# Kernel tuning notes

Hardware: AMD Instinct MI355X
Metric: run time of the kernel (lower is better)

The kernel has to match this reference:

```python
import jax, jax.numpy as jnp
import numpy as np
from jax import lax

NUM_MASKS = 100
NUM_CLASSES = 81  # 80 + 1
KERNEL_DIM = 256
BIAS_PRIOR = float(-np.log((1 - 0.01) / 0.01))


def setup_inputs() -> dict:
    key = jax.random.key(0)
    ks = jax.random.split(key, 12)
    B, C, H, W = 4, 256, 160, 160
    D = C  # expand_dim = in_channels * num_groups
    inp = {
        "features": jax.random.normal(ks[0], (B, C, H, W), jnp.float32),
        # iam_conv: Conv2d(C, num_masks, 3, padding=1)
        "w_iam": jax.random.normal(ks[1], (NUM_MASKS, C, 3, 3), jnp.float32) * 0.01,
        "b_iam": jnp.full((NUM_MASKS,), BIAS_PRIOR, jnp.float32),
        "softmax_bias": jnp.ones((1,), jnp.float32),
        # fc: Linear(D, D), xavier-ish
        "w_fc": jax.random.normal(ks[2], (D, D), jnp.float32) * (1.0 / np.sqrt(D)),
        "b_fc": jnp.zeros((D,), jnp.float32),
        "w_cls": jax.random.normal(ks[3], (NUM_CLASSES, D), jnp.float32) * 0.01,
        "b_cls": jnp.full((NUM_CLASSES,), BIAS_PRIOR, jnp.float32),
        "w_ker": jax.random.normal(ks[4], (KERNEL_DIM, D), jnp.float32) * 0.01,
        "b_ker": jnp.zeros((KERNEL_DIM,), jnp.float32),
        "w_obj": jax.random.normal(ks[5], (1, D), jnp.float32) * (1.0 / np.sqrt(D)),
        "b_obj": jnp.zeros((1,), jnp.float32),
        "w_box": jax.random.normal(ks[6], (4, D), jnp.float32) * 0.01,
        "b_box": jnp.zeros((4,), jnp.float32),
    }
    return inp


def reference(features, w_iam, b_iam, softmax_bias, w_fc, b_fc,
              w_cls, b_cls, w_ker, b_ker, w_obj, b_obj, w_box, b_box):
    B, C, H, W = features.shape
    # conv score map: (B, num_masks, H, W)
    iam = lax.conv_general_dilated(
        features, w_iam, window_strides=(1, 1), padding="SAME",
        dimension_numbers=("NCHW", "OIHW", "NCHW")) + b_iam[None, :, None, None]
    # num_groups == 1: single group iam
    iam_flat = iam.reshape(B, NUM_MASKS, H * W)
    # softmax over HW with learned scalar bias (bias shifts uniformly -> no-op math-wise but kept faithful)
    iam_prob = jax.nn.softmax(iam_flat + softmax_bias[0], axis=-1)  # (B, M, HW)
    # spatial attention pooling: bmm(prob, feats^T) -> (B, M, C)
    inst = jnp.einsum("bmp,bcp->bmc", iam_prob, features.reshape(B, C, H * W))
    # prev_inst_features is None -> skip fc_fuse
    inst = jax.nn.relu(inst @ w_fc.T + b_fc)
    pred_logits = inst @ w_cls.T + b_cls
    pred_kernel = inst @ w_ker.T + b_ker
    pred_scores = inst @ w_obj.T + b_obj
    pred_bboxes = inst @ w_box.T + b_box
    return (pred_logits, pred_kernel, pred_scores, pred_bboxes, iam, inst)
```

## Files before the change

kernel.cpp:

```cpp
#include <hip/hip_runtime.h>
#include <hip/hip_bf16.h>

typedef __attribute__((ext_vector_type(8))) short bf16x8;
typedef __attribute__((ext_vector_type(4))) float f32x4;

#define HW_ 25600
#define HP_ 162
#define WP_ 162

__device__ __forceinline__ unsigned short f2bf(float f) {
    __bf16 h = (__bf16)f;
    return *(unsigned short*)&h;
}
__device__ __forceinline__ float bf2f(unsigned short v) {
    union { unsigned u; float f; } x; x.u = ((unsigned)v) << 16;
    return x.f;
}

typedef const __attribute__((address_space(1))) unsigned int* gas_t;
typedef __attribute__((address_space(3))) unsigned int* las_t;
__device__ __forceinline__ void gl_lds16(const void* g, void* l) {
    __builtin_amdgcn_global_load_lds((gas_t)g, (las_t)l, 16, 0, 0);
}

__global__ __launch_bounds__(256) void k_prepcvt(const float* __restrict__ w_iam,
                                                 unsigned short* __restrict__ wp,
                                                 const float* __restrict__ feat,
                                                 unsigned short* __restrict__ fpad) {
    int bid = blockIdx.x;
    if (bid < 1152) {
        int idx = bid * 256 + threadIdx.x;
        int stage = idx >> 12;
        int r = idx & 4095;
        int m = r >> 5, cl = r & 31;
        int tap = stage >> 3, kc = stage & 7;
        int jj = (cl >> 3) ^ ((m >> 1) & 3);
        int c = kc * 32 + jj * 8 + (cl & 7);
        int dy = (tap * 11) >> 5, dx = tap - dy * 3;
        float v = (m < 100) ? w_iam[((m * 256 + c) * 3 + dy) * 3 + dx] : 0.f;
        wp[idx] = f2bf(v);
    } else if (bid < 3728) {
        int idx = (bid - 1152) * 256 + threadIdx.x;
        const int perb = 164864;
        if (idx >= 4 * perb) return;
        int b = idx / perb;
        int r = idx - b * perb;
        int hp, wpp, c;
        if (r < 82944) {
            hp = (r < 41472) ? 0 : 161;
            int r2 = r % 41472;
            wpp = r2 >> 8; c = r2 & 255;
        } else {
            r -= 82944;
            wpp = (r < 40960) ? 0 : 161;
            int r2 = r % 40960;
            hp = 1 + (r2 >> 8); c = r2 & 255;
        }
        fpad[((b * HP_ + hp) * WP_ + wpp) * 256 + c] = 0;
    } else {
        int cb = bid - 3728;
        int b = cb / 640;
        int h = (cb >> 2) % 160;
        int c0 = (cb & 3) * 64;
        __shared__ float tile[64][161];
        int t = threadIdx.x;
        const float4* src4 = (const float4*)(feat + ((long)(b * 256 + c0) * 160 + h) * 160);
        #pragma unroll
        for (int s = 0; s < 10; ++s) {
            int q = t + s * 256;
            int ci = q / 40;
            int w4 = q - ci * 40;
            float4 v = src4[(long)ci * 6400 + w4];
            tile[ci][w4 * 4 + 0] = v.x;
            tile[ci][w4 * 4 + 1] = v.y;
            tile[ci][w4 * 4 + 2] = v.z;
            tile[ci][w4 * 4 + 3] = v.w;
        }
        __syncthreads();
        int co = (t & 7) * 8, wq = t >> 3;
        unsigned short* dst = fpad + ((long)(b * HP_ + h + 1) * WP_ + 1) * 256 + c0 + co;
        #pragma unroll
        for (int wp2 = 0; wp2 < 5; ++wp2) {
            int w = wq + wp2 * 32;
            bf16x8 v;
            #pragma unroll
            for (int j = 0; j < 8; ++j) v[j] = (short)f2bf(tile[co + j][w]);
            *(bf16x8*)(dst + (long)w * 256) = v;
        }
    }
}

__global__ __launch_bounds__(512, 4) void k_conv(const unsigned short* __restrict__ fpad,
                                                 const unsigned short* __restrict__ wprep,
                                                 const float* __restrict__ b_iam,
                                                 float* __restrict__ iam) {
    int bid = blockIdx.x;
    bid = (bid & 7) * 50 + (bid >> 3);
    int b = bid / 100;
    int p0 = (bid % 100) * 256;
    int tid = threadIdx.x;
    int lane = tid & 63, wid = tid >> 6;
    int wr = wid >> 2, wc = wid & 3;

    __shared__ __align__(16) char smem[24576 + 2 * 17408];

    int h0 = p0 / 160, w0 = p0 - h0 * 160;
    int istar1 = 160 - w0, istar2 = 320 - w0;
    const unsigned short* fb = fpad + (long)b * HP_ * WP_ * 256;

    long rt0, rt1, rt2;
    {
        int c = tid & 3;
        int r0 = tid >> 2;
        rt0 = (long)r0 * 256 + ((c ^ ((r0 >> 1) & 3)) << 3);
        int r1 = 128 + (tid >> 2);
        rt1 = (long)r1 * 256 + ((c ^ ((r1 >> 1) & 3)) << 3);
        int r2 = 256 + (lane >> 2);
        int c2 = lane & 3;
        rt2 = (long)r2 * 256 + ((c2 ^ ((r2 >> 1) & 3)) << 3);
    }

    f32x4 acc[4][4];
    #pragma unroll
    for (int i = 0; i < 4; ++i)
        #pragma unroll
        for (int j = 0; j < 4; ++j)
            #pragma unroll
            for (int k = 0; k < 4; ++k) acc[i][j][k] = 0.f;

    int aBase = (wr << 12) + ((lane & 15) << 6) + ((((lane >> 4) ^ ((lane >> 1) & 3))) << 4);
    int rb[4];
    #pragma unroll
    for (int nf = 0; nf < 4; ++nf) {
        int i = wc * 64 + nf * 16 + (lane & 15);
        rb[nf] = i + 2 * (i >= istar1) + 2 * (i >= istar2);
    }

    auto issueA = [&](int s) {
        int dy = s >> 3, kc = s & 7;
        #pragma unroll
        for (int dx = 0; dx < 3; ++dx) {
            const unsigned short* ga = wprep + ((long)((dy * 3 + dx) * 8 + kc) << 12) + (tid << 3);
            gl_lds16(ga, smem + (dx << 13) + (wid << 10));
        }
    };
    auto issueB = [&](int s, int bi) {
        int dy = s >> 3, kc = s & 7;
        char* Bd = smem + 24576 + bi * 17408;
        long base = ((long)((h0 + dy) * WP_ + w0)) * 256 + (kc << 5);
        gl_lds16(fb + base + rt0, Bd + (wid << 10));
        gl_lds16(fb + base + rt1, Bd + 8192 + (wid << 10));
        if (wid == 0) gl_lds16(fb + base + rt2, Bd + 16384);
    };

    auto compute = [&](int bi) {
        const char* Ab = smem;
        const char* Bb = smem + 24576 + bi * 17408;
        #pragma unroll
        for (int dx = 0; dx < 3; ++dx) {
            bf16x8 af[4], bfv[4];
            #pragma unroll
            for (int mf = 0; mf < 4; ++mf)
                af[mf] = *(const bf16x8*)(Ab + (dx << 13) + aBase + (mf << 10));
            #pragma unroll
            for (int nf = 0; nf < 4; ++nf) {
                int row = rb[nf] + dx;
                bfv[nf] = *(const bf16x8*)(Bb + (row << 6) +
                            ((((lane >> 4) ^ ((row >> 1) & 3))) << 4));
            }
            __builtin_amdgcn_s_setprio(1);
            #pragma unroll
            for (int mf = 0; mf < 4; ++mf)
                #pragma unroll
                for (int nf = 0; nf < 4; ++nf)
                    acc[mf][nf] = __builtin_amdgcn_mfma_f32_16x16x32_bf16(
                        af[mf], bfv[nf], acc[mf][nf], 0, 0, 0);
            __builtin_amdgcn_s_setprio(0);
        }
    };

    issueB(0, 0);
    issueA(0);
    for (int s = 0; s < 24; ++s) {
        if (s < 23) {
            issueB(s + 1, (s + 1) & 1);
            if (wid == 0) asm volatile("s_waitcnt vmcnt(3)" ::: "memory");
            else          asm volatile("s_waitcnt vmcnt(2)" ::: "memory");
        } else {
            asm volatile("s_waitcnt vmcnt(0)" ::: "memory");
        }
        __builtin_amdgcn_sched_barrier(0);
        __builtin_amdgcn_s_barrier();
        __builtin_amdgcn_sched_barrier(0);
        compute(s & 1);
        __builtin_amdgcn_sched_barrier(0);
        __builtin_amdgcn_s_barrier();
        __builtin_amdgcn_sched_barrier(0);
        if (s < 23) issueA(s + 1);
    }

    float* dst = iam + (long)b * 100 * HW_;
    #pragma unroll
    for (int mf = 0; mf < 4; ++mf)
        #pragma unroll
        for (int nf = 0; nf < 4; ++nf) {
            int p = p0 + wc * 64 + nf * 16 + (lane & 15);
            int m0 = wr * 64 + mf * 16 + ((lane >> 4) << 2);
            #pragma unroll
            for (int j = 0; j < 4; ++j) {
                int m = m0 + j;
                if (m < 100) dst[(long)m * HW_ + p] = acc[mf][nf][j] + b_iam[m];
            }
        }
}

__global__ __launch_bounds__(512, 2) void k_pool(const float* __restrict__ feat,
                                                 const float* __restrict__ iam,
                                                 unsigned short* __restrict__ partials,
                                                 float* __restrict__ psum) {
    int bid = blockIdx.x;
    int b = bid / 100;
    int sl = bid - b * 100;
    int p0 = sl * 256;
    int tid = threadIdx.x, lane = tid & 63, wid = tid >> 6;
    int wm = wid >> 2, wcq = wid & 3;

    __shared__ __align__(16) unsigned short A[128 * 72];
    __shared__ __align__(16) unsigned short Bl[256 * 72];
    __shared__ float sums[128];
    if (tid < 128) sums[tid] = 0.f;
    __syncthreads();

    f32x4 acc[4][4];
    #pragma unroll
    for (int i = 0; i < 4; ++i)
        #pragma unroll
        for (int j = 0; j < 4; ++j)
            #pragma unroll
            for (int k = 0; k < 4; ++k) acc[i][j][k] = 0.f;

    int kgrp = (lane >> 4) << 3;

    for (int ks = 0; ks < 4; ++ks) {
        int k0 = p0 + ks * 64;
        #pragma unroll
        for (int s = 0; s < 2; ++s) {
            int q = tid + s * 512;
            int mi = q >> 3, j0 = (q & 7) * 8;
            bf16x8 o;
            if (mi < 100) {
                const float4* sp4 = (const float4*)(iam + (long)(b * 100 + mi) * HW_ + k0 + j0);
                float4 v0 = sp4[0], v1 = sp4[1];
                float xv[8] = {v0.x, v0.y, v0.z, v0.w, v1.x, v1.y, v1.z, v1.w};
                float ls = 0.f;
                #pragma unroll
                for (int j = 0; j < 8; ++j) {
                    float e = __expf(xv[j]);
                    o[j] = (short)f2bf(e);
                    ls += e;
                }
                atomicAdd(&sums[mi], ls);
            } else {
                #pragma unroll
                for (int j = 0; j < 8; ++j) o[j] = 0;
            }
            *(bf16x8*)(A + mi * 72 + j0) = o;
        }
        #pragma unroll
        for (int s = 0; s < 4; ++s) {
            int q = tid + s * 512;
            int ci = q >> 3, j0 = (q & 7) * 8;
            const float4* sp4 = (const float4*)(feat + (long)(b * 256 + ci) * HW_ + k0 + j0);
            float4 v0 = sp4[0], v1 = sp4[1];
            float xv[8] = {v0.x, v0.y, v0.z, v0.w, v1.x, v1.y, v1.z, v1.w};
            bf16x8 o;
            #pragma unroll
            for (int j = 0; j < 8; ++j) o[j] = (short)f2bf(xv[j]);
            *(bf16x8*)(Bl + ci * 72 + j0) = o;
        }
        __syncthreads();
        #pragma unroll
        for (int kk = 0; kk < 64; kk += 32) {
            bf16x8 af[4], bfv[4];
            #pragma unroll
            for (int mf = 0; mf < 4; ++mf)
                af[mf] = *(const bf16x8*)(A + (wm * 64 + mf * 16 + (lane & 15)) * 72 + kk + kgrp);
            #pragma unroll
            for (int nf = 0; nf < 4; ++nf)
                bfv[nf] = *(const bf16x8*)(Bl + (wcq * 64 + nf * 16 + (lane & 15)) * 72 + kk + kgrp);
            #pragma unroll
            for (int mf = 0; mf < 4; ++mf)
                #pragma unroll
                for (int nf = 0; nf < 4; ++nf)
                    acc[mf][nf] = __builtin_amdgcn_mfma_f32_16x16x32_bf16(
                        af[mf], bfv[nf], acc[mf][nf], 0, 0, 0);
        }
        __syncthreads();
    }
    if (tid < 100) psum[(long)bid * 112 + tid] = sums[tid];
    unsigned short* dst = partials + (long)bid * 112 * 256;
    #pragma unroll
    for (int mf = 0; mf < 4; ++mf)
        #pragma unroll
        for (int nf = 0; nf < 4; ++nf) {
            int m0 = wm * 64 + mf * 16 + ((lane >> 4) << 2);
            int c  = wcq * 64 + nf * 16 + (lane & 15);
            #pragma unroll
            for (int j = 0; j < 4; ++j) {
                int m = m0 + j;
                if (m < 112) dst[(long)m * 256 + c] = f2bf(acc[mf][nf][j]);
            }
        }
}

__global__ __launch_bounds__(256) void k_redfc(const unsigned short* __restrict__ partials,
                                               const float* __restrict__ psum,
                                               const float* __restrict__ w_fc, const float* __restrict__ b_fc,
                                               const float* __restrict__ w_cls, const float* __restrict__ b_cls,
                                               const float* __restrict__ w_ker, const float* __restrict__ b_ker,
                                               const float* __restrict__ w_obj, const float* __restrict__ b_obj,
                                               const float* __restrict__ w_box, const float* __restrict__ b_box,
                                               float* __restrict__ out) {
    int r = blockIdx.x;
    int b = r / 100, m = r - b * 100;
    int t = threadIdx.x;
    __shared__ float red[256];
    __shared__ float row[256];
    __shared__ float inst_s[256];

    red[t] = (t < 100) ? psum[(long)(b * 100 + t) * 112 + m] : 0.f;
    __syncthreads();
    for (int o = 128; o > 0; o >>= 1) {
        if (t < o) red[t] += red[t + o];
        __syncthreads();
    }
    float d = red[0];

    float s = 0.f;
    for (int sl = 0; sl < 100; ++sl)
        s += bf2f(partials[((long)(b * 100 + sl) * 112 + m) * 256 + t]);
    row[t] = s / d;
    __syncthreads();
    {
        float acc = b_fc[t];
        const float4* wv = (const float4*)(w_fc + (long)t * 256);
        for (int c = 0; c < 64; ++c) {
            float4 w4 = wv[c];
            acc += w4.x * row[c * 4] + w4.y * row[c * 4 + 1] + w4.z * row[c * 4 + 2] + w4.w * row[c * 4 + 3];
        }
        acc = fmaxf(acc, 0.f);
        inst_s[t] = acc;
        out[10376800 + (long)r * 256 + t] = acc;
    }
    __syncthreads();
    {
        float acc = b_ker[t];
        const float4* wv = (const float4*)(w_ker + (long)t * 256);
        for (int c = 0; c < 64; ++c) {
            float4 w4 = wv[c];
            acc += w4.x * inst_s[c * 4] + w4.y * inst_s[c * 4 + 1] + w4.z * inst_s[c * 4 + 2] + w4.w * inst_s[c * 4 + 3];
        }
        out[32400 + (long)r * 256 + t] = acc;
    }
    if (t < 81) {
        float acc = b_cls[t];
        const float4* wv = (const float4*)(w_cls + (long)t * 256);
        for (int c = 0; c < 64; ++c) {
            float4 w4 = wv[c];
            acc += w4.x * inst_s[c * 4] + w4.y * inst_s[c * 4 + 1] + w4.z * inst_s[c * 4 + 2] + w4.w * inst_s[c * 4 + 3];
        }
        out[(long)r * 81 + t] = acc;
    }
    if (t == 0) {
        float acc = b_obj[0];
        for (int c = 0; c < 256; ++c) acc += w_obj[c] * inst_s[c];
        out[134800 + r] = acc;
    }
    if (t >= 1 && t < 5) {
        int j = t - 1;
        float acc = b_box[j];
        for (int c = 0; c < 256; ++c) acc += w_box[j * 256 + c] * inst_s[c];
        out[135200 + (long)r * 4 + j] = acc;
    }
}

extern "C" void kernel_launch(void* const* d_in, const int* in_sizes, int n_in,
                              void* d_out, int out_size, void* d_ws, size_t ws_size,
                              hipStream_t stream) {
    const float* feat  = (const float*)d_in[0];
    const float* w_iam = (const float*)d_in[1];
    const float* b_iam = (const float*)d_in[2];
    const float* w_fc  = (const float*)d_in[4];
    const float* b_fc  = (const float*)d_in[5];
    const float* w_cls = (const float*)d_in[6];
    const float* b_cls = (const float*)d_in[7];
    const float* w_ker = (const float*)d_in[8];
    const float* b_ker = (const float*)d_in[9];
    const float* w_obj = (const float*)d_in[10];
    const float* b_obj = (const float*)d_in[11];
    const float* w_box = (const float*)d_in[12];
    const float* b_box = (const float*)d_in[13];
    float* out = (float*)d_out;

    char* ws = (char*)d_ws;
    unsigned short* fpad  = (unsigned short*)ws;
    unsigned short* wprep = (unsigned short*)(ws + 53747712);
    float* iam = out + 136800;

    unsigned short* partials = (unsigned short*)ws;
    float* psum              = (float*)(ws + 22937600);

    k_prepcvt<<<dim3(6288), dim3(256), 0, stream>>>(w_iam, wprep, feat, fpad);
    k_conv   <<<dim3(400),  dim3(512), 0, stream>>>(fpad, wprep, b_iam, iam);
    k_pool   <<<dim3(400),  dim3(512), 0, stream>>>(feat, iam, partials, psum);
    k_redfc  <<<dim3(400),  dim3(256), 0, stream>>>(partials, psum, w_fc, b_fc, w_cls, b_cls,
                                                    w_ker, b_ker, w_obj, b_obj, w_box, b_box, out);
}
```

Before: 179.3 us.

## Fuse softmax-exp and attention pooling into conv epilogue, drop separate pool kernel

The conv kernel's epilogue now computes exp of the score map directly from accumulators, reduces row sums with shuffles, stages the bf16 exp values into shared memory, and runs the pooling MFMA GEMM against converted features in the same block. This removes the k_pool launch and its re-read of the fp32 iam map from global memory. Partials and psum move to a separate workspace region because fpad is still live during conv. The change also swaps in a manual round-to-nearest-even bf16 conversion and raises MFMA issue priority. In exchange, register pressure in the conv kernel goes up and the pool stage now runs at conv's occupancy.

```diff
diff --git a/kernel.cpp b/kernel.cpp
--- a/kernel.cpp
+++ b/kernel.cpp
@@ -3,14 +3,16 @@
 
 typedef __attribute__((ext_vector_type(8))) short bf16x8;
 typedef __attribute__((ext_vector_type(4))) float f32x4;
+typedef __attribute__((ext_vector_type(4))) short short4v;
 
 #define HW_ 25600
 #define HP_ 162
 #define WP_ 162
 
 __device__ __forceinline__ unsigned short f2bf(float f) {
-    __bf16 h = (__bf16)f;
-    return *(unsigned short*)&h;
+    union { float f; unsigned u; } x; x.f = f;
+    unsigned r = x.u + 0x7FFFu + ((x.u >> 16) & 1u);
+    return (unsigned short)(r >> 16);
 }
 __device__ __forceinline__ float bf2f(unsigned short v) {
     union { unsigned u; float f; } x; x.u = ((unsigned)v) << 16;
@@ -93,11 +95,15 @@
 __global__ __launch_bounds__(512, 4) void k_conv(const unsigned short* __restrict__ fpad,
                                                  const unsigned short* __restrict__ wprep,
                                                  const float* __restrict__ b_iam,
-                                                 float* __restrict__ iam) {
+                                                 float* __restrict__ iam,
+                                                 const float* __restrict__ feat,
+                                                 unsigned short* __restrict__ partials,
+                                                 float* __restrict__ psum) {
     int bid = blockIdx.x;
     bid = (bid & 7) * 50 + (bid >> 3);
     int b = bid / 100;
-    int p0 = (bid % 100) * 256;
+    int sl = bid % 100;
+    int p0 = sl * 256;
     int tid = threadIdx.x;
     int lane = tid & 63, wid = tid >> 6;
     int wr = wid >> 2, wc = wid & 3;
@@ -199,84 +205,88 @@
         if (s < 23) issueA(s + 1);
     }
 
+    unsigned short* Apool = (unsigned short*)smem;
+    unsigned short* Bpool = (unsigned short*)(smem + 18432);
+    float* sums = (float*)(smem + 55296);
+
+    if (tid < 128) sums[tid] = 0.f;
+    __syncthreads();
+
     float* dst = iam + (long)b * 100 * HW_;
+    unsigned int ebf[4][4][2];
     #pragma unroll
-    for (int mf = 0; mf < 4; ++mf)
+    for (int mf = 0; mf < 4; ++mf) {
+        float ls[4] = {0.f, 0.f, 0.f, 0.f};
         #pragma unroll
         for (int nf = 0; nf < 4; ++nf) {
             int p = p0 + wc * 64 + nf * 16 + (lane & 15);
             int m0 = wr * 64 + mf * 16 + ((lane >> 4) << 2);
+            float e[4];
             #pragma unroll
             for (int j = 0; j < 4; ++j) {
                 int m = m0 + j;
-                if (m < 100) dst[(long)m * HW_ + p] = acc[mf][nf][j] + b_iam[m];
+                float ev = 0.f;
+                if (m < 100) {
+                    float v = acc[mf][nf][j] + b_iam[m];
+                    dst[(long)m * HW_ + p] = v;
+                    ev = __expf(v);
+                }
+                e[j] = ev;
+                ls[j] += ev;
             }
-        }
-}
-
-__global__ __launch_bounds__(512, 2) void k_pool(const float* __restrict__ feat,
-                                                 const float* __restrict__ iam,
-                                                 unsigned short* __restrict__ partials,
-                                                 float* __restrict__ psum) {
-    int bid = blockIdx.x;
-    int b = bid / 100;
-    int sl = bid - b * 100;
-    int p0 = sl * 256;
-    int tid = threadIdx.x, lane = tid & 63, wid = tid >> 6;
-    int wm = wid >> 2, wcq = wid & 3;
-
-    __shared__ __align__(16) unsigned short A[128 * 72];
-    __shared__ __align__(16) unsigned short Bl[256 * 72];
-    __shared__ float sums[128];
-    if (tid < 128) sums[tid] = 0.f;
-    __syncthreads();
-
-    f32x4 acc[4][4];
+            ebf[mf][nf][0] = (unsigned)f2bf(e[0]) | ((unsigned)f2bf(e[1]) << 16);
+            ebf[mf][nf][1] = (unsigned)f2bf(e[2]) | ((unsigned)f2bf(e[3]) << 16);
+        }
+        #pragma unroll
+        for (int j = 0; j < 4; ++j) {
+            float r = ls[j];
+            r += __shfl_xor(r, 1); r += __shfl_xor(r, 2);
+            r += __shfl_xor(r, 4); r += __shfl_xor(r, 8);
+            if ((lane & 15) == 0) {
+                int m = wr * 64 + mf * 16 + ((lane >> 4) << 2) + j;
+                if (m < 100) atomicAdd(&sums[m], r);
+            }
+        }
+    }
+
+    f32x4 acc2[4][4];
     #pragma unroll
     for (int i = 0; i < 4; ++i)
         #pragma unroll
         for (int j = 0; j < 4; ++j)
             #pragma unroll
-            for (int k = 0; k < 4; ++k) acc[i][j][k] = 0.f;
+            for (int k = 0; k < 4; ++k) acc2[i][j][k] = 0.f;
 
     int kgrp = (lane >> 4) << 3;
 
     for (int ks = 0; ks < 4; ++ks) {
-        int k0 = p0 + ks * 64;
-        #pragma unroll
-        for (int s = 0; s < 2; ++s) {
-            int q = tid + s * 512;
-            int mi = q >> 3, j0 = (q & 7) * 8;
-            bf16x8 o;
-            if (mi < 100) {
-                const float4* sp4 = (const float4*)(iam + (long)(b * 100 + mi) * HW_ + k0 + j0);
-                float4 v0 = sp4[0], v1 = sp4[1];
-                float xv[8] = {v0.x, v0.y, v0.z, v0.w, v1.x, v1.y, v1.z, v1.w};
-                float ls = 0.f;
+        if (wc == ks) {
+            #pragma unroll
+            for (int mf = 0; mf < 4; ++mf)
                 #pragma unroll
-                for (int j = 0; j < 8; ++j) {
-                    float e = __expf(xv[j]);
-                    o[j] = (short)f2bf(e);
-                    ls += e;
+                for (int nf = 0; nf < 4; ++nf) {
+                    int pl = nf * 16 + (lane & 15);
+                    int m0 = wr * 64 + mf * 16 + ((lane >> 4) << 2);
+                    #pragma unroll
+                    for (int pr = 0; pr < 2; ++pr) {
+                        unsigned w = ebf[mf][nf][pr];
+                        Apool[(m0 + pr * 2) * 72 + pl]     = (unsigned short)(w & 0xFFFF);
+                        Apool[(m0 + pr * 2 + 1) * 72 + pl] = (unsigned short)(w >> 16);
+                    }
                 }
-                atomicAdd(&sums[mi], ls);
-            } else {
-                #pragma unroll
-                for (int j = 0; j < 8; ++j) o[j] = 0;
+        }
+        {
+            int kp0 = p0 + ks * 64;
+            #pragma unroll
+            for (int s = 0; s < 8; ++s) {
+                int slot = tid + s * 512;
+                int c = slot >> 4, f4 = slot & 15;
+                float4 v = *(const float4*)(feat + (long)(b * 256 + c) * HW_ + kp0 + f4 * 4);
+                short4v o;
+                o.x = (short)f2bf(v.x); o.y = (short)f2bf(v.y);
+                o.z = (short)f2bf(v.z); o.w = (short)f2bf(v.w);
+                *(short4v*)(Bpool + c * 72 + f4 * 4) = o;
             }
-            *(bf16x8*)(A + mi * 72 + j0) = o;
-        }
-        #pragma unroll
-        for (int s = 0; s < 4; ++s) {
-            int q = tid + s * 512;
-            int ci = q >> 3, j0 = (q & 7) * 8;
-            const float4* sp4 = (const float4*)(feat + (long)(b * 256 + ci) * HW_ + k0 + j0);
-            float4 v0 = sp4[0], v1 = sp4[1];
-            float xv[8] = {v0.x, v0.y, v0.z, v0.w, v1.x, v1.y, v1.z, v1.w};
-            bf16x8 o;
-            #pragma unroll
-            for (int j = 0; j < 8; ++j) o[j] = (short)f2bf(xv[j]);
-            *(bf16x8*)(Bl + ci * 72 + j0) = o;
         }
         __syncthreads();
         #pragma unroll
@@ -284,33 +294,36 @@
             bf16x8 af[4], bfv[4];
             #pragma unroll
             for (int mf = 0; mf < 4; ++mf)
-                af[mf] = *(const bf16x8*)(A + (wm * 64 + mf * 16 + (lane & 15)) * 72 + kk + kgrp);
+                af[mf] = *(const bf16x8*)(Apool + (wr * 64 + mf * 16 + (lane & 15)) * 72 + kk + kgrp);
             #pragma unroll
             for (int nf = 0; nf < 4; ++nf)
-                bfv[nf] = *(const bf16x8*)(Bl + (wcq * 64 + nf * 16 + (lane & 15)) * 72 + kk + kgrp);
+                bfv[nf] = *(const bf16x8*)(Bpool + (wc * 64 + nf * 16 + (lane & 15)) * 72 + kk + kgrp);
+            __builtin_amdgcn_s_setprio(1);
             #pragma unroll
             for (int mf = 0; mf < 4; ++mf)
                 #pragma unroll
                 for (int nf = 0; nf < 4; ++nf)
-                    acc[mf][nf] = __builtin_amdgcn_mfma_f32_16x16x32_bf16(
-                        af[mf], bfv[nf], acc[mf][nf], 0, 0, 0);
+                    acc2[mf][nf] = __builtin_amdgcn_mfma_f32_16x16x32_bf16(
+                        af[mf], bfv[nf], acc2[mf][nf], 0, 0, 0);
+            __builtin_amdgcn_s_setprio(0);
         }
         __syncthreads();
     }
-    if (tid < 100) psum[(long)bid * 112 + tid] = sums[tid];
-    unsigned short* dst = partials + (long)bid * 112 * 256;
+
+    unsigned short* pdst = partials + (long)(b * 100 + sl) * 112 * 256;
     #pragma unroll
     for (int mf = 0; mf < 4; ++mf)
         #pragma unroll
         for (int nf = 0; nf < 4; ++nf) {
-            int m0 = wm * 64 + mf * 16 + ((lane >> 4) << 2);
-            int c  = wcq * 64 + nf * 16 + (lane & 15);
+            int m0 = wr * 64 + mf * 16 + ((lane >> 4) << 2);
+            int c  = wc * 64 + nf * 16 + (lane & 15);
             #pragma unroll
             for (int j = 0; j < 4; ++j) {
                 int m = m0 + j;
-                if (m < 112) dst[(long)m * 256 + c] = f2bf(acc[mf][nf][j]);
+                if (m < 112) pdst[(long)m * 256 + c] = f2bf(acc2[mf][nf][j]);
             }
         }
+    if (tid < 100) psum[(long)(b * 100 + sl) * 112 + tid] = sums[tid];
 }
 
 __global__ __launch_bounds__(256) void k_redfc(const unsigned short* __restrict__ partials,
@@ -405,14 +418,12 @@
     char* ws = (char*)d_ws;
     unsigned short* fpad  = (unsigned short*)ws;
     unsigned short* wprep = (unsigned short*)(ws + 53747712);
+    unsigned short* partials = (unsigned short*)(ws + 54337536);
+    float* psum              = (float*)(ws + 77275136);
     float* iam = out + 136800;
 
-    unsigned short* partials = (unsigned short*)ws;
-    float* psum              = (float*)(ws + 22937600);
-
     k_prepcvt<<<dim3(6288), dim3(256), 0, stream>>>(w_iam, wprep, feat, fpad);
-    k_conv   <<<dim3(400),  dim3(512), 0, stream>>>(fpad, wprep, b_iam, iam);
-    k_pool   <<<dim3(400),  dim3(512), 0, stream>>>(feat, iam, partials, psum);
+    k_conv   <<<dim3(400),  dim3(512), 0, stream>>>(fpad, wprep, b_iam, iam, feat, partials, psum);
     k_redfc  <<<dim3(400),  dim3(256), 0, stream>>>(partials, psum, w_fc, b_fc, w_cls, b_cls,
                                                     w_ker, b_ker, w_obj, b_obj, w_box, b_box, out);
 }
```

Measured after the change: 271.0 us. +51.2%, slower.
